# Kernel optimization log

Measured on AMD Instinct MI355X. Metric: run time of the kernel, lower is better.

## Reference

```python
import jax, jax.numpy as jnp
import numpy as np

V = 32000   # input_size (vocab)
H = 768     # hidden_size
C = 256     # condition_size
HC = H + C  # h_c_size
L = 2048    # sequence length


def _lstm_step(x, h, c, W_ih, W_hh, b_ih, b_hh):
    # PyTorch LSTM gate order: i, f, g, o
    gates = x @ W_ih.T + b_ih + h @ W_hh.T + b_hh  # [4*HC]
    i, f, g, o = jnp.split(gates, 4)
    c_new = jax.nn.sigmoid(f) * c + jax.nn.sigmoid(i) * jnp.tanh(g)
    h_new = jax.nn.sigmoid(o) * jnp.tanh(c_new)
    return h_new, c_new


def setup_inputs() -> dict:
    key = jax.random.key(0)
    ks = iter(jax.random.split(key, 40))
    p = lambda shape: (jax.random.normal(next(ks), shape, dtype=jnp.float32) * 0.02)
    inp = {
        "input": jax.random.randint(next(ks), (1, L), 0, V, dtype=jnp.int64),
        "condition": jax.random.randint(next(ks), (1,), 0, 4, dtype=jnp.int64),
        "eps_h": jax.random.normal(next(ks), (H,), dtype=jnp.float32),
        "eps_c": jax.random.normal(next(ks), (H,), dtype=jnp.float32),
        "kld_weight": jax.random.uniform(next(ks), (1,), dtype=jnp.float32),
        # encoder params
        "enc_embed": p((V, HC)),
        "enc_cond_embed": p((4, C)),
        "enc_W_ih": p((4 * HC, HC)), "enc_W_hh": p((4 * HC, HC)),
        "enc_b_ih": p((4 * HC,)), "enc_b_hh": p((4 * HC,)),
        "fc_mh_w": p((H, HC)), "fc_mh_b": p((H,)),
        "fc_lh_w": p((H, HC)), "fc_lh_b": p((H,)),
        "fc_mc_w": p((H, HC)), "fc_mc_b": p((H,)),
        "fc_lc_w": p((H, HC)), "fc_lc_b": p((H,)),
        # decoder params
        "dec_embed": p((V, HC)),
        "dec_cond_embed": p((4, C)),
        "dec_W_ih": p((4 * HC, HC)), "dec_W_hh": p((4 * HC, HC)),
        "dec_b_ih": p((4 * HC,)), "dec_b_hh": p((4 * HC,)),
        "fc_h_w": p((H, HC)), "fc_h_b": p((H,)),
        "fc_c_w": p((H, HC)), "fc_c_b": p((H,)),
        "out_w": p((V, HC)), "out_b": p((V,)),
    }
    return inp


def reference(input, condition, eps_h, eps_c, kld_weight,
              enc_embed, enc_cond_embed, enc_W_ih, enc_W_hh, enc_b_ih, enc_b_hh,
              fc_mh_w, fc_mh_b, fc_lh_w, fc_lh_b, fc_mc_w, fc_mc_b, fc_lc_w, fc_lc_b,
              dec_embed, dec_cond_embed, dec_W_ih, dec_W_hh, dec_b_ih, dec_b_hh,
              fc_h_w, fc_h_b, fc_c_w, fc_c_b, out_w, out_b):
    tokens = input[0]          # [L]
    cond = condition[0]

    # ---- Encoder over tokens[1:-1] ----
    x_seq = enc_embed[tokens[1:-1]]              # [L-2, HC]
    c_emb = enc_cond_embed[cond]                 # [C]
    h0 = jnp.concatenate([jnp.zeros((H,), jnp.float32), c_emb])  # [HC]
    c0 = h0

    def enc_step(carry, x):
        h, c = carry
        h, c = _lstm_step(x, h, c, enc_W_ih, enc_W_hh, enc_b_ih, enc_b_hh)
        return (h, c), None

    (hT, cT), _ = jax.lax.scan(enc_step, (h0, c0), x_seq)

    m_h = hT @ fc_mh_w.T + fc_mh_b
    lv_h = hT @ fc_lh_w.T + fc_lh_b
    z_h = eps_h * jnp.exp(lv_h * 0.5) + m_h      # [H]
    m_c = cT @ fc_mc_w.T + fc_mc_b
    lv_c = cT @ fc_lc_w.T + fc_lc_b
    z_c = eps_c * jnp.exp(lv_c * 0.5) + m_c

    kl_h = 0.5 * jnp.sum(m_h ** 2 + jnp.exp(lv_h) - 1.0 - lv_h)
    kl_c = 0.5 * jnp.sum(m_c ** 2 + jnp.exp(lv_c) - 1.0 - lv_c)

    # ---- Decoder, teacher forcing over L-1 steps ----
    dec_x = dec_embed[tokens[:-1]]               # [L-1, HC]
    targets = tokens[1:]                         # [L-1]
    cd = dec_cond_embed[cond]                    # [C]

    def dec_step(carry, xt):
        h, c = carry                             # [H], [H]
        x, tgt = xt
        hc = jnp.concatenate([h, cd])            # [HC]
        cc = jnp.concatenate([c, cd])
        h_new, c_new = _lstm_step(x, hc, cc, dec_W_ih, dec_W_hh, dec_b_ih, dec_b_hh)
        logits = h_new @ out_w.T + out_b         # [V]
        ce = -jax.nn.log_softmax(logits)[tgt]
        h2 = h_new @ fc_h_w.T + fc_h_b
        c2 = c_new @ fc_c_w.T + fc_c_b
        return (h2, c2), ce

    _, ces = jax.lax.scan(dec_step, (z_h, z_c), (dec_x, targets))
    reconst = jnp.mean(ces)
    loss = reconst + (kl_h + kl_c) * kld_weight[0]
    return jnp.stack([loss, reconst, kl_h, kl_c])
```

## Files before the change

### kernel.cpp

```cpp
#include <hip/hip_runtime.h>
#include <math.h>

#define VSZ 32000
#define Hh  768
#define Cc  256
#define HCd 1024
#define G4  4096
#define NSE 2046
#define NSD 2047

#define EB 64
#define ET 512
#define FGRID 256

typedef __attribute__((ext_vector_type(4))) unsigned uint4v;
typedef __attribute__((ext_vector_type(2))) unsigned uint2v;
typedef __attribute__((ext_vector_type(8))) short bf16x8;
typedef __attribute__((ext_vector_type(4))) float f32x4;

__device__ __forceinline__ float sigmoidf_(float x){ return 1.0f/(1.0f+expf(-x)); }

__device__ __forceinline__ float wave_reduce(float v){
#pragma unroll
  for(int o=32;o;o>>=1) v += __shfl_xor(v,o,64);
  return v;
}
__device__ __forceinline__ float redl0(float v){
  int x;
  x=__builtin_amdgcn_update_dpp(0,__float_as_int(v),0xB1,0xf,0xf,true); v+=__int_as_float(x);
  x=__builtin_amdgcn_update_dpp(0,__float_as_int(v),0x4E,0xf,0xf,true); v+=__int_as_float(x);
  v+=__int_as_float(__builtin_amdgcn_ds_swizzle(__float_as_int(v),0x101F));
  v+=__int_as_float(__builtin_amdgcn_ds_swizzle(__float_as_int(v),0x201F));
  v+=__int_as_float(__builtin_amdgcn_ds_swizzle(__float_as_int(v),0x401F));
  v+=__int_as_float(__builtin_amdgcn_readlane(__float_as_int(v),32));
  return v;
}

__device__ __forceinline__ uint2v ld_uc2(const unsigned* p){
  uint2v r;
  asm volatile("global_load_dwordx2 %0, %1, off sc0 sc1\n\ts_waitcnt vmcnt(0)"
               : "=v"(r) : "v"(p) : "memory");
  return r;
}
__device__ __forceinline__ uint4v ld_uc4(const unsigned* p){
  uint4v r;
  asm volatile("global_load_dwordx4 %0, %1, off sc0 sc1\n\ts_waitcnt vmcnt(0)"
               : "=v"(r) : "v"(p) : "memory");
  return r;
}
__device__ __forceinline__ void st_uc2(unsigned* p, uint2v v){
  asm volatile("global_store_dwordx2 %0, %1, off sc0 sc1" :: "v"(p), "v"(v) : "memory");
}
__device__ __forceinline__ void st_uc4(unsigned* p, uint4v v){
  asm volatile("global_store_dwordx4 %0, %1, off sc0 sc1" :: "v"(p), "v"(v) : "memory");
}

__device__ __forceinline__ unsigned pk_bf16(float a, float b){
  unsigned ua=__float_as_uint(a); ua += 0x7fffu + ((ua>>16)&1u);
  unsigned ub=__float_as_uint(b); ub += 0x7fffu + ((ub>>16)&1u);
  return (ua>>16) | (ub & 0xffff0000u);
}

__global__ void k_init9(unsigned* estate, unsigned* dstate,
                        const float* __restrict__ cemb, const int* __restrict__ condp){
  int tid=threadIdx.x;
  int cond=condp[0];
  for(int i=tid;i<HCd;i+=256){
    float v=(i<Hh)?0.f:cemb[cond*Cc+(i-Hh)];
    estate[i]=__float_as_uint(v)&~1u;
    estate[HCd+i]=1u;
  }
  for(int i=tid;i<2*HCd;i+=256) dstate[i]=0u;
}

#define GBM 128
#define GBN 128
#define GBK 16
#define TBM 128
#define TBN 128
#define TBK 32

struct SmU {
  union {
    float hlds[2][HCd];
    struct { float As[GBK][GBM]; float Bs[GBK][GBN]; } wf;
    struct { ushort As[TBM*TBK]; ushort Bs[TBN*TBK]; } xd;
  } u;
};

__device__ void weff_unit(int u, const float* __restrict__ A,
    const float* __restrict__ B, float* __restrict__ Cm, SmU& sm, int tid){
  int m0=(u>>3)*GBM, n0=(u&7)*GBN;
  int tm=tid>>4, tn=tid&15;
  float acc[8][8]={};
  for(int k0=0;k0<Hh;k0+=GBK){
    if(tid<256){
#pragma unroll
      for(int uu=0;uu<2;uu++){
        int idx=tid*2+uu;
        int row=idx>>2, q=idx&3;
        float4 v=*(const float4*)(A+(size_t)(m0+row)*HCd + k0+q*4);
        sm.u.wf.As[q*4+0][row]=v.x; sm.u.wf.As[q*4+1][row]=v.y;
        sm.u.wf.As[q*4+2][row]=v.z; sm.u.wf.As[q*4+3][row]=v.w;
        int kk=idx>>5, nc=idx&31;
        float4 w=*(const float4*)(B+(size_t)(k0+kk)*HCd + n0+nc*4);
        *(float4*)&sm.u.wf.Bs[kk][nc*4]=w;
      }
    }
    __syncthreads();
    if(tid<256){
#pragma unroll
      for(int kk=0;kk<GBK;kk++){
        float a[8],b[8];
        *(float4*)&a[0]=*(float4*)&sm.u.wf.As[kk][tm*8]; *(float4*)&a[4]=*(float4*)&sm.u.wf.As[kk][tm*8+4];
        *(float4*)&b[0]=*(float4*)&sm.u.wf.Bs[kk][tn*8]; *(float4*)&b[4]=*(float4*)&sm.u.wf.Bs[kk][tn*8+4];
#pragma unroll
        for(int i=0;i<8;i++)
#pragma unroll
          for(int j=0;j<8;j++) acc[i][j]+=a[i]*b[j];
      }
    }
    __syncthreads();
  }
  if(tid<256){
#pragma unroll
    for(int i=0;i<8;i++)
#pragma unroll
      for(int j=0;j<8;j++)
        Cm[(size_t)(m0+tm*8+i)*HCd + n0+tn*8+j]=acc[i][j];
  }
}

__device__ void xdec_unit(int q, const float* __restrict__ emb,
    const float* __restrict__ Wih, const float* __restrict__ b1,
    const float* __restrict__ b2, const int* __restrict__ tok,
    float* __restrict__ X, SmU& sm, int tid){
  int m0=(q>>5)*TBM, n0=(q&31)*TBN;
  int wid=tid>>6, lane=tid&63;
  int wm=wid>>1, wn=wid&1;
  int r15=lane&15, g=lane>>4;
  f32x4 acc[4][4]={};
  int srow=tid>>1, shalf=tid&1;
  int arow=m0+srow;
  bool act=(tid<256);
  int atok=(act&&arow<NSD)?tok[arow]:0;
  const float* aptr=emb+(size_t)atok*HCd + shalf*16;
  const float* bptr=Wih+(size_t)(n0+srow)*HCd + shalf*16;
  bool aok=act&&(arow<NSD);
  float bj[4];
  if(act){
#pragma unroll
    for(int j=0;j<4;j++){ int n=n0+wn*64+j*16+r15; bj[j]=b1[n]+b2[n]; }
  }
  for(int k0=0;k0<HCd;k0+=TBK){
    if(act){
      float4 va0={0,0,0,0},va1={0,0,0,0},va2={0,0,0,0},va3={0,0,0,0};
      if(aok){
        va0=*(const float4*)(aptr+k0);   va1=*(const float4*)(aptr+k0+4);
        va2=*(const float4*)(aptr+k0+8); va3=*(const float4*)(aptr+k0+12);
      }
      float4 vb0=*(const float4*)(bptr+k0),   vb1=*(const float4*)(bptr+k0+4);
      float4 vb2=*(const float4*)(bptr+k0+8), vb3=*(const float4*)(bptr+k0+12);
      uint4v pa0={pk_bf16(va0.x,va0.y),pk_bf16(va0.z,va0.w),pk_bf16(va1.x,va1.y),pk_bf16(va1.z,va1.w)};
      uint4v pa1={pk_bf16(va2.x,va2.y),pk_bf16(va2.z,va2.w),pk_bf16(va3.x,va3.y),pk_bf16(va3.z,va3.w)};
      uint4v pb0={pk_bf16(vb0.x,vb0.y),pk_bf16(vb0.z,vb0.w),pk_bf16(vb1.x,vb1.y),pk_bf16(vb1.z,vb1.w)};
      uint4v pb1={pk_bf16(vb2.x,vb2.y),pk_bf16(vb2.z,vb2.w),pk_bf16(vb3.x,vb3.y),pk_bf16(vb3.z,vb3.w)};
      int sx=(srow>>1)&3;
      int u0=(shalf*2+0)^sx, u1=(shalf*2+1)^sx;
      *(uint4v*)&sm.u.xd.As[srow*32+u0*8]=pa0; *(uint4v*)&sm.u.xd.As[srow*32+u1*8]=pa1;
      *(uint4v*)&sm.u.xd.Bs[srow*32+u0*8]=pb0; *(uint4v*)&sm.u.xd.Bs[srow*32+u1*8]=pb1;
    }
    __syncthreads();
    if(act){
      bf16x8 af[4], bf[4];
#pragma unroll
      for(int i=0;i<4;i++){
        int ra=wm*64+i*16+r15;
        af[i]=*(const bf16x8*)&sm.u.xd.As[ra*32+((g^((ra>>1)&3))<<3)];
        int rb=wn*64+i*16+r15;
        bf[i]=*(const bf16x8*)&sm.u.xd.Bs[rb*32+((g^((rb>>1)&3))<<3)];
      }
#pragma unroll
      for(int i=0;i<4;i++)
#pragma unroll
        for(int j=0;j<4;j++)
          acc[i][j]=__builtin_amdgcn_mfma_f32_16x16x32_bf16(af[i],bf[j],acc[i][j],0,0,0);
    }
    __syncthreads();
  }
  if(act){
#pragma unroll
    for(int i=0;i<4;i++){
      int grow0=m0+wm*64+i*16+g*4;
#pragma unroll
      for(int j=0;j<4;j++){
        int gcol=n0+wn*64+j*16+r15;
#pragma unroll
        for(int r=0;r<4;r++){
          int grow=grow0+r;
          if(grow<NSD) X[(size_t)grow*G4+gcol]=acc[i][j][r]+bj[j];
        }
      }
    }
  }
}

__device__ void cvtb_unit(int i, const float* __restrict__ B,
    unsigned* __restrict__ Bb, int tid){
  size_t base=(size_t)i*128000u;
  for(size_t x=base+tid; x<base+128000u; x+=ET){
    float4 v=*(const float4*)(B+x*4);
    Bb[x*2]  =pk_bf16(v.x,v.y);
    Bb[x*2+1]=pk_bf16(v.z,v.w);
  }
}

__device__ void dconst_unit(int i, const float* __restrict__ Whh,
    const float* __restrict__ fhb, const float* __restrict__ cemb,
    int cond, float* __restrict__ cvec, int tid){
// ... 142 lines not shown
    int do_xdec, int do_cvtb)
{
  __shared__ SmU sm;
  const int tid=threadIdx.x, lane=tid&63, wv=tid>>6;
  const int bid=blockIdx.x;

  if(bid>=EB){
    int cond=condp[0];
    int n_x=do_xdec?512:0, n_c=do_cvtb?64:0;
    int total=16+256+n_x+n_c;
    for(int u=bid-EB; u<total; u+=FGRID-EB){
      if(u<16) dconst_unit(u,dWhh,fhb,dcemb,cond,cvec,tid);
      else if(u<272) weff_unit(u-16,dWhh,fhw,Weff,sm,tid);
      else if(u<272+n_x) xdec_unit(u-272,demb,dWih,dbih,dbhh,tok,XB,sm,tid);
      else cvtb_unit(u-272-n_x,outw,wB,tid);
      __syncthreads();
    }
    return;
  }

  const int wid=bid*8+wv;
  const int j0=wid*2, j1=j0+1;
  float w[8][16];
#pragma unroll
  for(int q=0;q<4;q++)
#pragma unroll
    for(int jj=0;jj<2;jj++){
      const float* p=Whh+(size_t)(q*HCd+j0+jj)*HCd+lane;
#pragma unroll
      for(int e=0;e<16;e++) w[q*2+jj][e]=p[(size_t)e*64];
    }
  float xg[8];
#pragma unroll
  for(int r=0;r<8;r++) xg[r]=Xg[(r>>1)*HCd+j0+(r&1)];
  float c0=0.f,c1=0.f;
  const int i0=tid*2, i1=i0+1;

  for(int s=1;s<=NSE;s++){
    uint2v v;
    unsigned* src=estate+((s-1)&1)*HCd;
    if(s==1){ v.x=src[i0]; v.y=src[i1]; }
    else{
      const unsigned expp=(unsigned)(((s-1)>>1)&1);
      for(;;){
        v=ld_uc2(src+i0);
        if((((v.x^expp)|(v.y^expp))&1u)==0u) break;
        __builtin_amdgcn_s_sleep(1);
      }
    }
    float* hl=sm.u.hlds[(s-1)&1];
    hl[i0]=__uint_as_float(v.x); hl[i1]=__uint_as_float(v.y);
    __syncthreads();
    if(s==1){ c0=hl[j0]; c1=hl[j1]; }
    float hseg[16];
#pragma unroll
    for(int e=0;e<16;e++) hseg[e]=hl[lane+64*e];
    float d[8];
#pragma unroll
    for(int r=0;r<8;r++){ float sacc=0.f;
#pragma unroll
      for(int e=0;e<16;e++) sacc+=w[r][e]*hseg[e];
      d[r]=sacc; }
#pragma unroll
    for(int r=0;r<8;r++) d[r]=redl0(d[r]);
    float gi0=d[0]+xg[0], gi1=d[1]+xg[1];
    float gf0=d[2]+xg[2], gf1=d[3]+xg[3];
    float gg0=d[4]+xg[4], gg1=d[5]+xg[5];
    float go0=d[6]+xg[6], go1=d[7]+xg[7];
    if(s<NSE){
      const float* px=Xg+(size_t)s*G4;
#pragma unroll
      for(int r=0;r<8;r++) xg[r]=px[(r>>1)*HCd+j0+(r&1)];
    }
    c0=sigmoidf_(gf0)*c0+sigmoidf_(gi0)*tanhf(gg0);
    float h0=sigmoidf_(go0)*tanhf(c0);
    c1=sigmoidf_(gf1)*c1+sigmoidf_(gi1)*tanhf(gg1);
    float h1=sigmoidf_(go1)*tanhf(c1);
    unsigned wpar=(unsigned)((s>>1)&1);
    if(lane==0){
      uint2v pk;
      pk.x=(__float_as_uint(h0)&~1u)|wpar;
      pk.y=(__float_as_uint(h1)&~1u)|wpar;
      st_uc2(estate+(s&1)*HCd+j0,pk);
      if(s==NSE){ hT[j0]=h0; hT[j1]=h1; cT[j0]=c0; cT[j1]=c1; }
    }
  }
}

__global__ __launch_bounds__(256) void k_head(
    const float* __restrict__ hT, const float* __restrict__ cT,
    const float* __restrict__ mhw, const float* __restrict__ mhb,
    const float* __restrict__ lhw, const float* __restrict__ lhb,
    const float* __restrict__ mcw, const float* __restrict__ mcb,
    const float* __restrict__ lcw, const float* __restrict__ lcb,
    const float* __restrict__ eps_h, const float* __restrict__ eps_c,
    const float* __restrict__ cemb, const int* __restrict__ condp,
    float* zh, float* zc, float* klh, float* klc)
{
  int i=blockIdx.x;
  int tid=threadIdx.x, lane=tid&63, wv=tid>>6;
  __shared__ float sm[4];
  const float* Wm=(wv==0)?mhw:(wv==1)?lhw:(wv==2)?mcw:lcw;
  const float* vec=(wv<2)?hT:cT;
  const float* row=Wm+(size_t)i*HCd;
  float s=0.f;
  for(int k=lane;k<HCd;k+=64) s+=row[k]*vec[k];
  s=wave_reduce(s);
  if(lane==0) sm[wv]=s;
  __syncthreads();
  if(tid==0){
    float mh=sm[0]+mhb[i], lh=sm[1]+lhb[i];
    float mc=sm[2]+mcb[i], lc=sm[3]+lcb[i];
    zh[i]=eps_h[i]*expf(lh*0.5f)+mh;
    zc[i]=eps_c[i]*expf(lc*0.5f)+mc;
    klh[i]=0.5f*(mh*mh+expf(lh)-1.f-lh);
    klc[i]=0.5f*(mc*mc+expf(lc)-1.f-lc);
    if(i<Cc){
      float cd=cemb[condp[0]*Cc+i];
      zh[Hh+i]=cd; zc[Hh+i]=cd;
    }
  }
}

__global__ __launch_bounds__(256) void k_dec0(
    const float* __restrict__ Xg, const float* __restrict__ WhhO,
    const float* __restrict__ zh, const float* __restrict__ zc,
    unsigned* dstate1, float* Hmat)
{
  int tid=threadIdx.x, lane=tid&63, wv=tid>>6;
  int j=blockIdx.x*4+wv;
  float hseg[16];
#pragma unroll
  for(int e=0;e<16;e++) hseg[e]=zh[lane+64*e];
  float g[4];
#pragma unroll
  for(int q=0;q<4;q++){
    const float* p=WhhO+(size_t)(q*HCd+j)*HCd+lane;
    float s=0.f;
#pragma unroll
    for(int e=0;e<16;e++) s+=p[(size_t)e*64]*hseg[e];
    s=wave_reduce(s);
    g[q]=s+Xg[q*HCd+j];
  }
  float cc=zc[j];
  float cn=sigmoidf_(g[1])*cc+sigmoidf_(g[0])*tanhf(g[2]);
  float hn=sigmoidf_(g[3])*tanhf(cn);
  if(lane==0){
    dstate1[2*j]  =__float_as_uint(hn)&~1u;
    dstate1[2*j+1]=__float_as_uint(cn)&~1u;
    Hmat[j]=hn;
  }
}

__global__ __launch_bounds__(ET,2) void k_dec9(
    const float* __restrict__ Xg, const float* __restrict__ Weff,
    const float* __restrict__ cvec,
    const float* __restrict__ fccw, const float* __restrict__ fccb,
    const float* __restrict__ cemb, const int* __restrict__ condp,
    unsigned* dstate, float* __restrict__ Hmat)
{
  __shared__ float hlds[2][HCd];
  __shared__ float clds[2][HCd];
  const int tid=threadIdx.x, lane=tid&63, wv=tid>>6;
  const int wid=blockIdx.x*8+wv;
  const int j0=wid*2, j1=j0+1;
  float w[8][16];
#pragma unroll
  for(int q=0;q<4;q++)
#pragma unroll
    for(int jj=0;jj<2;jj++){
      const float* p=Weff+(size_t)(q*HCd+j0+jj)*HCd+lane;
#pragma unroll
      for(int e=0;e<16;e++) w[q*2+jj][e]=p[(size_t)e*64];
    }
  const bool hasf=(j0<Hh);
  float fcc0[16], fcc1[16];
  if(hasf){
    const float* p0=fccw+(size_t)j0*HCd+lane;
    const float* p1=fccw+(size_t)j1*HCd+lane;
#pragma unroll
    for(int e=0;e<16;e++){ fcc0[e]=p0[(size_t)e*64]; fcc1[e]=p1[(size_t)e*64]; }
  } else {
#pragma unroll
    for(int e=0;e<16;e++){ fcc0[e]=0.f; fcc1[e]=0.f; }
  }
  float fb0=hasf?fccb[j0]:0.f, fb1=hasf?fccb[j1]:0.f;
  int cond=condp[0];
  float cd0=hasf?0.f:cemb[cond*Cc+(j0-Hh)];
  float cd1=hasf?0.f:cemb[cond*Cc+(j1-Hh)];
  float cv[8];
#pragma unroll
  for(int r=0;r<8;r++) cv[r]=cvec[(r>>1)*HCd+j0+(r&1)];
  float xg[8];
  { const float* px=Xg+(size_t)1*G4;
#pragma unroll
    for(int r=0;r<8;r++) xg[r]=px[(r>>1)*HCd+j0+(r&1)]; }
  const int i0=tid*2, i1=i0+1;

  for(int s=2;s<=NSD;s++){
    uint4v v;
    unsigned* st=dstate+((s-1)&1)*2*HCd;
    if(s==2){ v=*(const uint4v*)(st+4*tid); }
    else{
      const unsigned expp=(unsigned)(((s-1)>>1)&1);
      for(;;){
        v=ld_uc4(st+4*tid);
        if((((v.x^expp)|(v.y^expp)|(v.z^expp)|(v.w^expp))&1u)==0u) break;
        __builtin_amdgcn_s_sleep(1);
      }
    }
    float* hl=hlds[(s-1)&1]; float* cl=clds[(s-1)&1];
    hl[i0]=__uint_as_float(v.x); cl[i0]=__uint_as_float(v.y);
    hl[i1]=__uint_as_float(v.z); cl[i1]=__uint_as_float(v.w);
    __syncthreads();
    float hseg[16], cseg[16];
#pragma unroll
    for(int e=0;e<16;e++){ hseg[e]=hl[lane+64*e]; cseg[e]=cl[lane+64*e]; }
    float d[8]; float s8=0.f, s9=0.f;
#pragma unroll
    for(int r=0;r<8;r++){ float sacc=0.f;
#pragma unroll
      for(int e=0;e<16;e++) sacc+=w[r][e]*hseg[e];
      d[r]=sacc; }
#pragma unroll
    for(int r=0;r<8;r++) d[r]=redl0(d[r]);
    if(hasf){
#pragma unroll
      for(int e=0;e<16;e++){ s8+=fcc0[e]*cseg[e]; s9+=fcc1[e]*cseg[e]; }
      s8=redl0(s8); s9=redl0(s9);
    }
    float gi0=d[0]+xg[0]+cv[0], gi1=d[1]+xg[1]+cv[1];
    float gf0=d[2]+xg[2]+cv[2], gf1=d[3]+xg[3]+cv[3];
    float gg0=d[4]+xg[4]+cv[4], gg1=d[5]+xg[5]+cv[5];
    float go0=d[6]+xg[6]+cv[6], go1=d[7]+xg[7]+cv[7];
    if(s<NSD){
      const float* px=Xg+(size_t)s*G4;
#pragma unroll
      for(int r=0;r<8;r++) xg[r]=px[(r>>1)*HCd+j0+(r&1)];
    }
    float cc0=hasf?(s8+fb0):cd0;
    float cc1=hasf?(s9+fb1):cd1;
    float cn0=sigmoidf_(gf0)*cc0+sigmoidf_(gi0)*tanhf(gg0);
    float hn0=sigmoidf_(go0)*tanhf(cn0);
    float cn1=sigmoidf_(gf1)*cc1+sigmoidf_(gi1)*tanhf(gg1);
    float hn1=sigmoidf_(go1)*tanhf(cn1);
    unsigned wpar=(unsigned)((s>>1)&1);
    if(lane==0){
      uint4v pk;
      pk.x=(__float_as_uint(hn0)&~1u)|wpar;
      pk.y=(__float_as_uint(cn0)&~1u)|wpar;
      pk.z=(__float_as_uint(hn1)&~1u)|wpar;
      pk.w=(__float_as_uint(cn1)&~1u)|wpar;
      st_uc4(dstate+(s&1)*2*HCd+2*j0,pk);
      Hmat[(size_t)(s-1)*HCd+j0]=hn0; Hmat[(size_t)(s-1)*HCd+j1]=hn1;
    }
  }
}

__global__ __launch_bounds__(256) void k_gemm2(
    const float* __restrict__ A, const ushort* __restrict__ Bb,
    const float* __restrict__ bias, float* __restrict__ Cm, int M)
{
  __shared__ ushort As[TBM*TBK];
  __shared__ ushort Bs[TBN*TBK];
  int tid=threadIdx.x;
  int m0=blockIdx.x*TBM, n0=blockIdx.y*TBN;
  int wid=tid>>6, lane=tid&63;
  int wm=wid>>1, wn=wid&1;
  int r15=lane&15, g=lane>>4;
  f32x4 acc[4][4]={};
  int srow=tid>>1, shalf=tid&1;
  const float*  aptr=A +(size_t)(m0+srow)*HCd + shalf*16;
  const ushort* bptr=Bb+(size_t)(n0+srow)*HCd + shalf*16;
  bool aok=(m0+srow)<M;
  float bj[4];
#pragma unroll
  for(int j=0;j<4;j++) bj[j]=bias[n0+wn*64+j*16+r15];

  for(int k0=0;k0<HCd;k0+=TBK){
    float4 va0={0,0,0,0},va1={0,0,0,0},va2={0,0,0,0},va3={0,0,0,0};
    if(aok){
      va0=*(const float4*)(aptr+k0);   va1=*(const float4*)(aptr+k0+4);
      va2=*(const float4*)(aptr+k0+8); va3=*(const float4*)(aptr+k0+12);
    }
    uint4v qb0=*(const uint4v*)(bptr+k0);
    uint4v qb1=*(const uint4v*)(bptr+k0+8);
    uint4v pa0={pk_bf16(va0.x,va0.y),pk_bf16(va0.z,va0.w),pk_bf16(va1.x,va1.y),pk_bf16(va1.z,va1.w)};
    uint4v pa1={pk_bf16(va2.x,va2.y),pk_bf16(va2.z,va2.w),pk_bf16(va3.x,va3.y),pk_bf16(va3.z,va3.w)};
    int sx=(srow>>1)&3;
    int u0=(shalf*2+0)^sx, u1=(shalf*2+1)^sx;
    *(uint4v*)&As[srow*32+u0*8]=pa0; *(uint4v*)&As[srow*32+u1*8]=pa1;
    *(uint4v*)&Bs[srow*32+u0*8]=qb0; *(uint4v*)&Bs[srow*32+u1*8]=qb1;
    __syncthreads();
    bf16x8 af[4], bf[4];
#pragma unroll
    for(int i=0;i<4;i++){
      int ra=wm*64+i*16+r15;
      af[i]=*(const bf16x8*)&As[ra*32+((g^((ra>>1)&3))<<3)];
      int rb=wn*64+i*16+r15;
      bf[i]=*(const bf16x8*)&Bs[rb*32+((g^((rb>>1)&3))<<3)];
    }
#pragma unroll
    for(int i=0;i<4;i++)
#pragma unroll
      for(int j=0;j<4;j++)
        acc[i][j]=__builtin_amdgcn_mfma_f32_16x16x32_bf16(af[i],bf[j],acc[i][j],0,0,0);
    __syncthreads();
  }
#pragma unroll
  for(int i=0;i<4;i++){
    int grow0=m0+wm*64+i*16+g*4;
#pragma unroll
    for(int j=0;j<4;j++){
      int gcol=n0+wn*64+j*16+r15;
#pragma unroll
      for(int r=0;r<4;r++){
        int grow=grow0+r;
        if(grow<M) Cm[(size_t)grow*VSZ+gcol]=acc[i][j][r]+bj[j];
      }
    }
  }
}

__global__ __launch_bounds__(256) void k_gemm_mfma(
    const float* __restrict__ A, const float* __restrict__ B,
    const float* __restrict__ bias, float* __restrict__ Cm, int M)
{
  __shared__ ushort As[TBM*TBK];
  __shared__ ushort Bs[TBN*TBK];
  int tid=threadIdx.x;
  int m0=blockIdx.x*TBM, n0=blockIdx.y*TBN;
  int wid=tid>>6, lane=tid&63;
  int wm=wid>>1, wn=wid&1;
  int r15=lane&15, g=lane>>4;
  f32x4 acc[4][4]={};
  int srow=tid>>1, shalf=tid&1;
  const float* aptr=A+(size_t)(m0+srow)*HCd + shalf*16;
  const float* bptr=B+(size_t)(n0+srow)*HCd + shalf*16;
  bool aok=(m0+srow)<M;
  float bj[4];
#pragma unroll
  for(int j=0;j<4;j++) bj[j]=bias[n0+wn*64+j*16+r15];
  for(int k0=0;k0<HCd;k0+=TBK){
    float4 va0={0,0,0,0},va1={0,0,0,0},va2={0,0,0,0},va3={0,0,0,0};
    if(aok){
      va0=*(const float4*)(aptr+k0);   va1=*(const float4*)(aptr+k0+4);
      va2=*(const float4*)(aptr+k0+8); va3=*(const float4*)(aptr+k0+12);
    }
    float4 vb0=*(const float4*)(bptr+k0),   vb1=*(const float4*)(bptr+k0+4);
    float4 vb2=*(const float4*)(bptr+k0+8), vb3=*(const float4*)(bptr+k0+12);
    uint4v pa0={pk_bf16(va0.x,va0.y),pk_bf16(va0.z,va0.w),pk_bf16(va1.x,va1.y),pk_bf16(va1.z,va1.w)};
    uint4v pa1={pk_bf16(va2.x,va2.y),pk_bf16(va2.z,va2.w),pk_bf16(va3.x,va3.y),pk_bf16(va3.z,va3.w)};
    uint4v pb0={pk_bf16(vb0.x,vb0.y),pk_bf16(vb0.z,vb0.w),pk_bf16(vb1.x,vb1.y),pk_bf16(vb1.z,vb1.w)};
    uint4v pb1={pk_bf16(vb2.x,vb2.y),pk_bf16(vb2.z,vb2.w),pk_bf16(vb3.x,vb3.y),pk_bf16(vb3.z,vb3.w)};
    int sx=(srow>>1)&3;
    int u0=(shalf*2+0)^sx, u1=(shalf*2+1)^sx;
    *(uint4v*)&As[srow*32+u0*8]=pa0; *(uint4v*)&As[srow*32+u1*8]=pa1;
    *(uint4v*)&Bs[srow*32+u0*8]=pb0; *(uint4v*)&Bs[srow*32+u1*8]=pb1;
    __syncthreads();
    bf16x8 af[4], bf[4];
#pragma unroll
    for(int i=0;i<4;i++){
      int ra=wm*64+i*16+r15;
      af[i]=*(const bf16x8*)&As[ra*32+((g^((ra>>1)&3))<<3)];
      int rb=wn*64+i*16+r15;
      bf[i]=*(const bf16x8*)&Bs[rb*32+((g^((rb>>1)&3))<<3)];
    }
#pragma unroll
    for(int i=0;i<4;i++)
#pragma unroll
      for(int j=0;j<4;j++)
        acc[i][j]=__builtin_amdgcn_mfma_f32_16x16x32_bf16(af[i],bf[j],acc[i][j],0,0,0);
    __syncthreads();
  }
#pragma unroll
  for(int i=0;i<4;i++){
    int grow0=m0+wm*64+i*16+g*4;
#pragma unroll
    for(int j=0;j<4;j++){
      int gcol=n0+wn*64+j*16+r15;
#pragma unroll
      for(int r=0;r<4;r++){
        int grow=grow0+r;
        if(grow<M) Cm[(size_t)grow*VSZ+gcol]=acc[i][j][r]+bj[j];
      }
    }
  }
}

__global__ __launch_bounds__(256) void k_ce(const float* __restrict__ logits,
    const int* __restrict__ tok, int base, float* __restrict__ ce)
{
  int r=blockIdx.x;
  const float* row=logits+(size_t)r*VSZ;
  int tid=threadIdx.x, lane=tid&63, wv=tid>>6;
  float m=-1e30f, s=0.f;
  for(int i=tid;i<VSZ;i+=256){
    float v=row[i];
    if(v>m){ s=s*__expf(m-v)+1.f; m=v; }
    else s+=__expf(v-m);
  }
#pragma unroll
  for(int o=32;o;o>>=1){
    float mo=__shfl_xor(m,o,64), so=__shfl_xor(s,o,64);
    float mn=fmaxf(m,mo);
    s=s*__expf(m-mn)+so*__expf(mo-mn);
    m=mn;
  }
  __shared__ float smm[4], sms[4];
  if(lane==0){ smm[wv]=m; sms[wv]=s; }
  __syncthreads();
  if(tid==0){
    float M2=fmaxf(fmaxf(smm[0],smm[1]),fmaxf(smm[2],smm[3]));
    float S2=sms[0]*__expf(smm[0]-M2)+sms[1]*__expf(smm[1]-M2)
            +sms[2]*__expf(smm[2]-M2)+sms[3]*__expf(smm[3]-M2);
    int tgt=tok[base+r+1];
    ce[base+r]=M2+logf(S2)-row[tgt];
  }
}

__global__ __launch_bounds__(256) void k_final(const float* __restrict__ ce,
    const float* __restrict__ klh, const float* __restrict__ klc,
    const float* __restrict__ kldw, float* __restrict__ outp)
{
  int tid=threadIdx.x, lane=tid&63, wv=tid>>6;
  float s0=0,s1=0,s2=0;
  for(int i=tid;i<NSD;i+=256) s0+=ce[i];
  for(int i=tid;i<Hh;i+=256){ s1+=klh[i]; s2+=klc[i]; }
  s0=wave_reduce(s0); s1=wave_reduce(s1); s2=wave_reduce(s2);
  __shared__ float sm[3][4];
  if(lane==0){ sm[0][wv]=s0; sm[1][wv]=s1; sm[2][wv]=s2; }
  __syncthreads();
  if(tid==0){
    float ces=sm[0][0]+sm[0][1]+sm[0][2]+sm[0][3];
    float kh =sm[1][0]+sm[1][1]+sm[1][2]+sm[1][3];
    float kc =sm[2][0]+sm[2][1]+sm[2][2]+sm[2][3];
    float rec=ces/(float)NSD;
    outp[0]=rec+(kh+kc)*kldw[0];
    outp[1]=rec; outp[2]=kh; outp[3]=kc;
  }
}

extern "C" void kernel_launch(void* const* d_in, const int* in_sizes, int n_in,
                              void* d_out, int out_size, void* d_ws, size_t ws_size,
                              hipStream_t stream) {
  const int*   tok   =(const int*)  d_in[0];
  const int*   cond  =(const int*)  d_in[1];
  const float* eps_h =(const float*)d_in[2];
  const float* eps_c =(const float*)d_in[3];
  const float* kldw  =(const float*)d_in[4];
  const float* enc_embed=(const float*)d_in[5];
  const float* enc_cemb =(const float*)d_in[6];
  const float* enc_Wih  =(const float*)d_in[7];
  const float* enc_Whh  =(const float*)d_in[8];
  const float* enc_bih  =(const float*)d_in[9];
  const float* enc_bhh  =(const float*)d_in[10];
  const float* fc_mh_w=(const float*)d_in[11];
  const float* fc_mh_b=(const float*)d_in[12];
  const float* fc_lh_w=(const float*)d_in[13];
  const float* fc_lh_b=(const float*)d_in[14];
  const float* fc_mc_w=(const float*)d_in[15];
  const float* fc_mc_b=(const float*)d_in[16];
  const float* fc_lc_w=(const float*)d_in[17];
  const float* fc_lc_b=(const float*)d_in[18];
  const float* dec_embed=(const float*)d_in[19];
  const float* dec_cemb =(const float*)d_in[20];
  const float* dec_Wih  =(const float*)d_in[21];
  const float* dec_Whh  =(const float*)d_in[22];
  const float* dec_bih  =(const float*)d_in[23];
  const float* dec_bhh  =(const float*)d_in[24];
  const float* fc_h_w=(const float*)d_in[25];
  const float* fc_h_b=(const float*)d_in[26];
  const float* fc_c_w=(const float*)d_in[27];
  const float* fc_c_b=(const float*)d_in[28];
  const float* out_w=(const float*)d_in[29];
  const float* out_b=(const float*)d_in[30];

  float* ws=(float*)d_ws;
  size_t off=0;
  unsigned* estate=(unsigned*)(ws+off); off+=2*HCd;
  unsigned* dstate=(unsigned*)(ws+off); off+=4*HCd;
  float* cvec=ws+off; off+=G4;
  float* Weff=ws+off; off+=(size_t)G4*HCd;
  float* hT  =ws+off; off+=HCd;
  float* cT  =ws+off; off+=HCd;
  float* zh  =ws+off; off+=HCd;
  float* zc  =ws+off; off+=HCd;
  float* klh =ws+off; off+=Hh;
  float* klc =ws+off; off+=Hh;
  float* Hmat=ws+off; off+=(size_t)NSD*HCd;
  float* ce  =ws+off; off+=2048;
  size_t avail=ws_size/4;
  size_t xa_sz=(size_t)NSE*G4, xb_sz=(size_t)NSD*G4;
  size_t wb_sz=(size_t)VSZ*HCd/2;
  float* XA=ws+off;
  bool dual=(off+xa_sz+xb_sz)<=avail;
  float* XB=dual?(XA+xa_sz):XA;
  bool wbok=dual && (off+xa_sz+xb_sz+wb_sz)<=avail;
  unsigned* wB=(unsigned*)(XB+xb_sz);
  size_t region=(avail>off)?(avail-off):0;
  int chunk;
  if(dual){
    chunk=(int)((xa_sz+xb_sz)/(size_t)VSZ); if(chunk>512)chunk=512;
  } else {
    chunk=256;
    if((size_t)chunk*VSZ>region){ chunk=(int)(region/(size_t)VSZ); if(chunk<1)chunk=1; }
  }
  float* lbuf=XA;

  k_init9<<<1,256,0,stream>>>(estate,dstate,enc_cemb,cond);
  { dim3 g((NSE+GBM-1)/GBM, G4/GBN);
    k_xgemm<<<g,256,0,stream>>>(enc_embed,enc_Wih,enc_bih,enc_bhh,tok,1,NSE,XA); }
  k_encF<<<FGRID,ET,0,stream>>>(XA,enc_Whh,estate,hT,cT,
                                dec_Whh,fc_h_w,Weff,
                                dec_embed,dec_Wih,dec_bih,dec_bhh,tok,XB,
                                out_w,wB,fc_h_b,dec_cemb,cond,cvec,
                                dual?1:0, wbok?1:0);
  k_head<<<Hh,256,0,stream>>>(hT,cT,fc_mh_w,fc_mh_b,fc_lh_w,fc_lh_b,
                              fc_mc_w,fc_mc_b,fc_lc_w,fc_lc_b,
                              eps_h,eps_c,dec_cemb,cond,zh,zc,klh,klc);
  if(!dual){
    dim3 g((NSD+TBM-1)/TBM, G4/TBN);
    k_xgemm_mfma<<<g,256,0,stream>>>(dec_embed,dec_Wih,dec_bih,dec_bhh,tok,NSD,XB);
  }
  k_dec0<<<256,256,0,stream>>>(XB,dec_Whh,zh,zc,dstate+2*HCd,Hmat);
  k_dec9<<<EB,ET,0,stream>>>(XB,Weff,cvec,fc_c_w,fc_c_b,dec_cemb,cond,dstate,Hmat);
  for(int base=0;base<NSD;base+=chunk){
    int rows=NSD-base; if(rows>chunk) rows=chunk;
    dim3 g((rows+TBM-1)/TBM, VSZ/TBN);
    if(wbok) k_gemm2<<<g,256,0,stream>>>(Hmat+(size_t)base*HCd,(const ushort*)wB,out_b,lbuf,rows);
    else     k_gemm_mfma<<<g,256,0,stream>>>(Hmat+(size_t)base*HCd,out_w,out_b,lbuf,rows);
    k_ce<<<rows,256,0,stream>>>(lbuf,tok,base,ce);
  }
  k_final<<<1,256,0,stream>>>(ce,klh,klc,kldw,(float*)d_out);
}
```

Before: 13.53 ms.

## Overlap decoder scan with fused vocab GEMM and online softmax via progress flags

Replaces the sequential decoder recurrence kernel and the chunked vocab-projection GEMM plus CE kernels with one persistent kernel. The first 64 blocks run the recurrence and publish per-block progress counters. The remaining blocks spin on those counters and compute the output logits tiles for rows already finished. They fuse bias, target-logit extraction and a partial log-sum-exp per tile, so the full logits matrix is never written. A small merge kernel then combines the partial max and sum values into the cross-entropy. The gain depends on all 256 blocks being co-resident, and the GEMM blocks contend with the latency-critical scan for memory bandwidth.

```diff
diff --git a/kernel.cpp b/kernel.cpp
--- a/kernel.cpp
+++ b/kernel.cpp
@@ -12,6 +12,7 @@
 #define EB 64
 #define ET 512
 #define FGRID 256
+#define NCT 125
 
 typedef __attribute__((ext_vector_type(4))) unsigned uint4v;
 typedef __attribute__((ext_vector_type(2))) unsigned uint2v;
@@ -23,6 +24,11 @@
 __device__ __forceinline__ float wave_reduce(float v){
 #pragma unroll
   for(int o=32;o;o>>=1) v += __shfl_xor(v,o,64);
+  return v;
+}
+__device__ __forceinline__ unsigned wave_min_u(unsigned v){
+#pragma unroll
+  for(int o=32;o;o>>=1){ unsigned x=__shfl_xor(v,o,64); v=(x<v)?x:v; }
   return v;
 }
 __device__ __forceinline__ float redl0(float v){
@@ -36,6 +42,12 @@
   return v;
 }
 
+__device__ __forceinline__ unsigned ld_uc1(const unsigned* p){
+  unsigned r;
+  asm volatile("global_load_dword %0, %1, off sc0 sc1\n\ts_waitcnt vmcnt(0)"
+               : "=v"(r) : "v"(p) : "memory");
+  return r;
+}
 __device__ __forceinline__ uint2v ld_uc2(const unsigned* p){
   uint2v r;
   asm volatile("global_load_dwordx2 %0, %1, off sc0 sc1\n\ts_waitcnt vmcnt(0)"
@@ -48,6 +60,9 @@
                : "=v"(r) : "v"(p) : "memory");
   return r;
 }
+__device__ __forceinline__ void st_uc1(unsigned* p, unsigned v){
+  asm volatile("global_store_dword %0, %1, off sc0 sc1" :: "v"(p), "v"(v) : "memory");
+}
 __device__ __forceinline__ void st_uc2(unsigned* p, uint2v v){
   asm volatile("global_store_dwordx2 %0, %1, off sc0 sc1" :: "v"(p), "v"(v) : "memory");
 }
@@ -61,10 +76,11 @@
   return (ua>>16) | (ub & 0xffff0000u);
 }
 
-__global__ void k_init9(unsigned* estate, unsigned* dstate,
-                        const float* __restrict__ cemb, const int* __restrict__ condp){
+__global__ void k_init12(unsigned* prog, unsigned* estate, unsigned* dstate,
+                         const float* __restrict__ cemb, const int* __restrict__ condp){
   int tid=threadIdx.x;
   int cond=condp[0];
+  for(int i=tid;i<4096;i+=256) prog[i]=0u;
   for(int i=tid;i<HCd;i+=256){
     float v=(i<Hh)?0.f:cemb[cond*Cc+(i-Hh)];
     estate[i]=__float_as_uint(v)&~1u;
@@ -513,6 +529,244 @@
   }
 }
 
+struct SmD {
+  union {
+    struct { float hl[2][HCd]; float cl[2][HCd]; } scan;
+    struct { ushort As[128*32]; ushort Bs[256*32];
+             float smM[128][4]; float smL[128][4]; int tgt[128]; } h;
+  } u;
+};
+
+__global__ __launch_bounds__(ET) void k_decF(
+    const float* __restrict__ Xg, const float* __restrict__ Weff,
+    const float* __restrict__ cvec,
+    const float* __restrict__ fccw, const float* __restrict__ fccb,
+    const float* __restrict__ cemb, const int* __restrict__ condp,
+    unsigned* dstate, float* __restrict__ Hmat, unsigned* prog,
+    const ushort* __restrict__ wB, const float* __restrict__ outb,
+    const int* __restrict__ tok,
+    float* __restrict__ pm, float* __restrict__ pl, float* __restrict__ tgtlog)
+{
+  __shared__ SmD smem;
+  const int tid=threadIdx.x, lane=tid&63, wv=tid>>6;
+  const int bid=blockIdx.x;
+
+  if(bid<EB){
+    const int wid=bid*8+wv;
+    const int j0=wid*2, j1=j0+1;
+    float w[8][16];
+#pragma unroll
+    for(int q=0;q<4;q++)
+#pragma unroll
+      for(int jj=0;jj<2;jj++){
+        const float* p=Weff+(size_t)(q*HCd+j0+jj)*HCd+lane;
+#pragma unroll
+        for(int e=0;e<16;e++) w[q*2+jj][e]=p[(size_t)e*64];
+      }
+    const bool hasf=(j0<Hh);
+    float fcc0[16], fcc1[16];
+    if(hasf){
+      const float* p0=fccw+(size_t)j0*HCd+lane;
+      const float* p1=fccw+(size_t)j1*HCd+lane;
+#pragma unroll
+      for(int e=0;e<16;e++){ fcc0[e]=p0[(size_t)e*64]; fcc1[e]=p1[(size_t)e*64]; }
+    } else {
+#pragma unroll
+      for(int e=0;e<16;e++){ fcc0[e]=0.f; fcc1[e]=0.f; }
+    }
+    float fb0=hasf?fccb[j0]:0.f, fb1=hasf?fccb[j1]:0.f;
+    int cond=condp[0];
+    float cd0=hasf?0.f:cemb[cond*Cc+(j0-Hh)];
+    float cd1=hasf?0.f:cemb[cond*Cc+(j1-Hh)];
+    float cv[8];
+#pragma unroll
+    for(int r=0;r<8;r++) cv[r]=cvec[(r>>1)*HCd+j0+(r&1)];
+    float xg[8];
+    { const float* px=Xg+(size_t)1*G4;
+#pragma unroll
+      for(int r=0;r<8;r++) xg[r]=px[(r>>1)*HCd+j0+(r&1)]; }
+    const int i0=tid*2, i1=i0+1;
+
+    for(int s=2;s<=NSD;s++){
+      uint4v v;
+      unsigned* st=dstate+((s-1)&1)*2*HCd;
+      if(s==2){ v=*(const uint4v*)(st+4*tid); }
+      else{
+        const unsigned expp=(unsigned)(((s-1)>>1)&1);
+        for(;;){
+          v=ld_uc4(st+4*tid);
+          if((((v.x^expp)|(v.y^expp)|(v.z^expp)|(v.w^expp))&1u)==0u) break;
+          __builtin_amdgcn_s_sleep(1);
+        }
+      }
+      float* hl=smem.u.scan.hl[(s-1)&1]; float* cl=smem.u.scan.cl[(s-1)&1];
+      hl[i0]=__uint_as_float(v.x); cl[i0]=__uint_as_float(v.y);
+      hl[i1]=__uint_as_float(v.z); cl[i1]=__uint_as_float(v.w);
+      __syncthreads();
+      if(tid==0) st_uc1(prog+bid*64,(unsigned)(s-2));
+      float hseg[16], cseg[16];
+#pragma unroll
+      for(int e=0;e<16;e++){ hseg[e]=hl[lane+64*e]; cseg[e]=cl[lane+64*e]; }
+      float d[8]; float s8=0.f, s9=0.f;
+#pragma unroll
+      for(int r=0;r<8;r++){ float sacc=0.f;
+#pragma unroll
+        for(int e=0;e<16;e++) sacc+=w[r][e]*hseg[e];
+        d[r]=sacc; }
+#pragma unroll
+      for(int r=0;r<8;r++) d[r]=redl0(d[r]);
+      if(hasf){
+#pragma unroll
+        for(int e=0;e<16;e++){ s8+=fcc0[e]*cseg[e]; s9+=fcc1[e]*cseg[e]; }
+        s8=redl0(s8); s9=redl0(s9);
+      }
+      float gi0=d[0]+xg[0]+cv[0], gi1=d[1]+xg[1]+cv[1];
+      float gf0=d[2]+xg[2]+cv[2], gf1=d[3]+xg[3]+cv[3];
+      float gg0=d[4]+xg[4]+cv[4], gg1=d[5]+xg[5]+cv[5];
+      float go0=d[6]+xg[6]+cv[6], go1=d[7]+xg[7]+cv[7];
+      if(s<NSD){
+        const float* px=Xg+(size_t)s*G4;
+#pragma unroll
+        for(int r=0;r<8;r++) xg[r]=px[(r>>1)*HCd+j0+(r&1)];
+      }
+      float cc0=hasf?(s8+fb0):cd0;
+      float cc1=hasf?(s9+fb1):cd1;
+      float cn0=sigmoidf_(gf0)*cc0+sigmoidf_(gi0)*tanhf(gg0);
+      float hn0=sigmoidf_(go0)*tanhf(cn0);
+      float cn1=sigmoidf_(gf1)*cc1+sigmoidf_(gi1)*tanhf(gg1);
+      float hn1=sigmoidf_(go1)*tanhf(cn1);
+      unsigned wpar=(unsigned)((s>>1)&1);
+      if(lane==0){
+        uint4v pk;
+        pk.x=(__float_as_uint(hn0)&~1u)|wpar;
+        pk.y=(__float_as_uint(cn0)&~1u)|wpar;
+        pk.z=(__float_as_uint(hn1)&~1u)|wpar;
+        pk.w=(__float_as_uint(cn1)&~1u)|wpar;
+        st_uc4(dstate+(s&1)*2*HCd+2*j0,pk);
+        uint2v hm; hm.x=__float_as_uint(hn0); hm.y=__float_as_uint(hn1);
+        st_uc2((unsigned*)(Hmat+(size_t)(s-1)*HCd+j0),hm);
+      }
+    }
+    asm volatile("s_waitcnt vmcnt(0)");
+    __syncthreads();
+    if(tid==0) st_uc1(prog+bid*64,(unsigned)(NSD-1));
+    return;
+  }
+
+  const int hb=bid-EB;
+  const int wid=tid>>6;
+  const int r15=lane&15, g=lane>>4;
+  const int wm=wid>>2, wn=wid&3;
+  const int srA=tid>>2, shA=tid&3;
+  const int srB=tid>>1, shB=tid&1;
+
+  for(int u=hb; u<8*2*NCT; u+=FGRID-EB){
+    int chunk=u/(2*NCT), t=u%(2*NCT);
+    int rt=t/NCT, ct=t%NCT;
+    int m0=chunk*256+rt*128, n0=ct*256;
+    unsigned need=(unsigned)((m0+127<NSD)?(m0+127):(NSD-1));
+    if(wv==0){
+      for(;;){
+        unsigned pv=ld_uc1(prog+lane*64);
+        if(wave_min_u(pv)>=need) break;
+        __builtin_amdgcn_s_sleep(32);
+      }
+    }
+    if(tid<128){
+      int grow=m0+tid;
+      smem.u.h.tgt[tid]=(grow<NSD)?tok[grow+1]:-1;
+    }
+    __syncthreads();
+
+    f32x4 acc[4][4]={};
+    const float*  aptr=Hmat+(size_t)(m0+srA)*HCd + shA*8;
+    const ushort* bptr=wB  +(size_t)(n0+srB)*HCd + shB*16;
+    bool aok=(m0+srA)<NSD;
+    for(int k0=0;k0<HCd;k0+=32){
+      float4 va0={0,0,0,0}, va1={0,0,0,0};
+      if(aok){ va0=*(const float4*)(aptr+k0); va1=*(const float4*)(aptr+k0+4); }
+      uint4v pa={pk_bf16(va0.x,va0.y),pk_bf16(va0.z,va0.w),pk_bf16(va1.x,va1.y),pk_bf16(va1.z,va1.w)};
+      int sxA=(srA>>1)&3;
+      *(uint4v*)&smem.u.h.As[srA*32+(shA^sxA)*8]=pa;
+      uint4v qb0=*(const uint4v*)(bptr+k0);
+      uint4v qb1=*(const uint4v*)(bptr+k0+8);
+      int sxB=(srB>>1)&3;
+      int u0=(shB*2+0)^sxB, u1=(shB*2+1)^sxB;
+      *(uint4v*)&smem.u.h.Bs[srB*32+u0*8]=qb0;
+      *(uint4v*)&smem.u.h.Bs[srB*32+u1*8]=qb1;
+      __syncthreads();
+      bf16x8 af[4], bf[4];
+#pragma unroll
+      for(int i=0;i<4;i++){
+        int ra=wm*64+i*16+r15;
+        af[i]=*(const bf16x8*)&smem.u.h.As[ra*32+((g^((ra>>1)&3))<<3)];
+        int rb=wn*64+i*16+r15;
+        bf[i]=*(const bf16x8*)&smem.u.h.Bs[rb*32+((g^((rb>>1)&3))<<3)];
+      }
+#pragma unroll
+      for(int i=0;i<4;i++)
+#pragma unroll
+        for(int j=0;j<4;j++)
+          acc[i][j]=__builtin_amdgcn_mfma_f32_16x16x32_bf16(af[i],bf[j],acc[i][j],0,0,0);
+      __syncthreads();
+    }
+    float bj[4];
+#pragma unroll
+    for(int j=0;j<4;j++) bj[j]=outb[n0+wn*64+j*16+r15];
+#pragma unroll
+    for(int i=0;i<4;i++)
+#pragma unroll
+    for(int r=0;r<4;r++){
+      int rloc=wm*64+i*16+g*4+r;
+      int tg=smem.u.h.tgt[rloc];
+      float vv[4];
+#pragma unroll
+      for(int j=0;j<4;j++){
+        vv[j]=acc[i][j][r]+bj[j];
+        if(n0+wn*64+j*16+r15==tg) tgtlog[m0+rloc]=vv[j];
+      }
+      float mloc=fmaxf(fmaxf(vv[0],vv[1]),fmaxf(vv[2],vv[3]));
+      float lloc=__expf(vv[0]-mloc)+__expf(vv[1]-mloc)+__expf(vv[2]-mloc)+__expf(vv[3]-mloc);
+#pragma unroll
+      for(int o=1;o<16;o<<=1){
+        float mo=__shfl_xor(mloc,o,64), lo=__shfl_xor(lloc,o,64);
+        float mn=fmaxf(mloc,mo);
+        lloc=lloc*__expf(mloc-mn)+lo*__expf(mo-mn);
+        mloc=mn;
+      }
+      if(r15==0){ smem.u.h.smM[rloc][wn]=mloc; smem.u.h.smL[rloc][wn]=lloc; }
+    }
+    __syncthreads();
+    if(tid<128){
+      int grow=m0+tid;
+      if(grow<NSD){
+        float M=-3e38f;
+#pragma unroll
+        for(int q2=0;q2<4;q2++) M=fmaxf(M,smem.u.h.smM[tid][q2]);
+        float L=0.f;
+#pragma unroll
+        for(int q2=0;q2<4;q2++) L+=smem.u.h.smL[tid][q2]*__expf(smem.u.h.smM[tid][q2]-M);
+        pm[(size_t)grow*NCT+ct]=M;
+        pl[(size_t)grow*NCT+ct]=L;
+      }
+    }
+    __syncthreads();
+  }
+}
+
+__global__ __launch_bounds__(256) void k_cemerge(const float* __restrict__ pm,
+    const float* __restrict__ pl, const float* __restrict__ tgtlog,
+    float* __restrict__ ce)
+{
+  int grow=blockIdx.x*256+threadIdx.x;
+  if(grow>=NSD) return;
+  float M=-3e38f;
+  for(int c=0;c<NCT;c++) M=fmaxf(M,pm[(size_t)grow*NCT+c]);
+  float L=0.f;
+  for(int c=0;c<NCT;c++) L+=pl[(size_t)grow*NCT+c]*__expf(pm[(size_t)grow*NCT+c]-M);
+  ce[grow]=M+logf(L)-tgtlog[grow];
+}
+
 __global__ __launch_bounds__(ET,2) void k_dec9(
     const float* __restrict__ Xg, const float* __restrict__ Weff,
     const float* __restrict__ cvec,
@@ -614,71 +868,6 @@
       pk.w=(__float_as_uint(cn1)&~1u)|wpar;
       st_uc4(dstate+(s&1)*2*HCd+2*j0,pk);
       Hmat[(size_t)(s-1)*HCd+j0]=hn0; Hmat[(size_t)(s-1)*HCd+j1]=hn1;
-    }
-  }
-}
-
-__global__ __launch_bounds__(256) void k_gemm2(
-    const float* __restrict__ A, const ushort* __restrict__ Bb,
-    const float* __restrict__ bias, float* __restrict__ Cm, int M)
-{
-  __shared__ ushort As[TBM*TBK];
-  __shared__ ushort Bs[TBN*TBK];
-  int tid=threadIdx.x;
-  int m0=blockIdx.x*TBM, n0=blockIdx.y*TBN;
-  int wid=tid>>6, lane=tid&63;
-  int wm=wid>>1, wn=wid&1;
-  int r15=lane&15, g=lane>>4;
-  f32x4 acc[4][4]={};
-  int srow=tid>>1, shalf=tid&1;
-  const float*  aptr=A +(size_t)(m0+srow)*HCd + shalf*16;
-  const ushort* bptr=Bb+(size_t)(n0+srow)*HCd + shalf*16;
-  bool aok=(m0+srow)<M;
-  float bj[4];
-#pragma unroll
-  for(int j=0;j<4;j++) bj[j]=bias[n0+wn*64+j*16+r15];
-
-  for(int k0=0;k0<HCd;k0+=TBK){
-    float4 va0={0,0,0,0},va1={0,0,0,0},va2={0,0,0,0},va3={0,0,0,0};
-    if(aok){
-      va0=*(const float4*)(aptr+k0);   va1=*(const float4*)(aptr+k0+4);
-      va2=*(const float4*)(aptr+k0+8); va3=*(const float4*)(aptr+k0+12);
-    }
-    uint4v qb0=*(const uint4v*)(bptr+k0);
-    uint4v qb1=*(const uint4v*)(bptr+k0+8);
-    uint4v pa0={pk_bf16(va0.x,va0.y),pk_bf16(va0.z,va0.w),pk_bf16(va1.x,va1.y),pk_bf16(va1.z,va1.w)};
-    uint4v pa1={pk_bf16(va2.x,va2.y),pk_bf16(va2.z,va2.w),pk_bf16(va3.x,va3.y),pk_bf16(va3.z,va3.w)};
-    int sx=(srow>>1)&3;
-    int u0=(shalf*2+0)^sx, u1=(shalf*2+1)^sx;
-    *(uint4v*)&As[srow*32+u0*8]=pa0; *(uint4v*)&As[srow*32+u1*8]=pa1;
-    *(uint4v*)&Bs[srow*32+u0*8]=qb0; *(uint4v*)&Bs[srow*32+u1*8]=qb1;
-    __syncthreads();
-    bf16x8 af[4], bf[4];
-#pragma unroll
-    for(int i=0;i<4;i++){
-      int ra=wm*64+i*16+r15;
-      af[i]=*(const bf16x8*)&As[ra*32+((g^((ra>>1)&3))<<3)];
-      int rb=wn*64+i*16+r15;
-      bf[i]=*(const bf16x8*)&Bs[rb*32+((g^((rb>>1)&3))<<3)];
-    }
-#pragma unroll
-    for(int i=0;i<4;i++)
-#pragma unroll
-      for(int j=0;j<4;j++)
-        acc[i][j]=__builtin_amdgcn_mfma_f32_16x16x32_bf16(af[i],bf[j],acc[i][j],0,0,0);
-    __syncthreads();
-  }
-#pragma unroll
-  for(int i=0;i<4;i++){
-    int grow0=m0+wm*64+i*16+g*4;
-#pragma unroll
-    for(int j=0;j<4;j++){
-      int gcol=n0+wn*64+j*16+r15;
-#pragma unroll
-      for(int r=0;r<4;r++){
-        int grow=grow0+r;
-        if(grow<M) Cm[(size_t)grow*VSZ+gcol]=acc[i][j][r]+bj[j];
-      }
     }
   }
 }
@@ -839,6 +1028,7 @@
 
   float* ws=(float*)d_ws;
   size_t off=0;
+  unsigned* prog  =(unsigned*)(ws+off); off+=4096;
   unsigned* estate=(unsigned*)(ws+off); off+=2*HCd;
   unsigned* dstate=(unsigned*)(ws+off); off+=4*HCd;
   float* cvec=ws+off; off+=G4;
@@ -851,6 +1041,9 @@
   float* klc =ws+off; off+=Hh;
   float* Hmat=ws+off; off+=(size_t)NSD*HCd;
   float* ce  =ws+off; off+=2048;
+  float* pm  =ws+off; off+=(size_t)2048*NCT;
+  float* pl  =ws+off; off+=(size_t)2048*NCT;
+  float* tgtlog=ws+off; off+=2048;
   size_t avail=ws_size/4;
   size_t xa_sz=(size_t)NSE*G4, xb_sz=(size_t)NSD*G4;
   size_t wb_sz=(size_t)VSZ*HCd/2;
@@ -860,16 +1053,13 @@
   bool wbok=dual && (off+xa_sz+xb_sz+wb_sz)<=avail;
   unsigned* wB=(unsigned*)(XB+xb_sz);
   size_t region=(avail>off)?(avail-off):0;
-  int chunk;
-  if(dual){
-    chunk=(int)((xa_sz+xb_sz)/(size_t)VSZ); if(chunk>512)chunk=512;
-  } else {
-    chunk=256;
+  int chunk=256;
+  if(!dual){
     if((size_t)chunk*VSZ>region){ chunk=(int)(region/(size_t)VSZ); if(chunk<1)chunk=1; }
   }
   float* lbuf=XA;
 
-  k_init9<<<1,256,0,stream>>>(estate,dstate,enc_cemb,cond);
+  k_init12<<<1,256,0,stream>>>(prog,estate,dstate,enc_cemb,cond);
   { dim3 g((NSE+GBM-1)/GBM, G4/GBN);
     k_xgemm<<<g,256,0,stream>>>(enc_embed,enc_Wih,enc_bih,enc_bhh,tok,1,NSE,XA); }
   k_encF<<<FGRID,ET,0,stream>>>(XA,enc_Whh,estate,hT,cT,
@@ -885,13 +1075,19 @@
     k_xgemm_mfma<<<g,256,0,stream>>>(dec_embed,dec_Wih,dec_bih,dec_bhh,tok,NSD,XB);
   }
   k_dec0<<<256,256,0,stream>>>(XB,dec_Whh,zh,zc,dstate+2*HCd,Hmat);
-  k_dec9<<<EB,ET,0,stream>>>(XB,Weff,cvec,fc_c_w,fc_c_b,dec_cemb,cond,dstate,Hmat);
-  for(int base=0;base<NSD;base+=chunk){
-    int rows=NSD-base; if(rows>chunk) rows=chunk;
-    dim3 g((rows+TBM-1)/TBM, VSZ/TBN);
-    if(wbok) k_gemm2<<<g,256,0,stream>>>(Hmat+(size_t)base*HCd,(const ushort*)wB,out_b,lbuf,rows);
-    else     k_gemm_mfma<<<g,256,0,stream>>>(Hmat+(size_t)base*HCd,out_w,out_b,lbuf,rows);
-    k_ce<<<rows,256,0,stream>>>(lbuf,tok,base,ce);
+  if(dual&&wbok){
+    k_decF<<<FGRID,ET,0,stream>>>(XB,Weff,cvec,fc_c_w,fc_c_b,dec_cemb,cond,
+                                  dstate,Hmat,prog,(const ushort*)wB,out_b,tok,
+                                  pm,pl,tgtlog);
+    k_cemerge<<<(NSD+255)/256,256,0,stream>>>(pm,pl,tgtlog,ce);
+  } else {
+    k_dec9<<<EB,ET,0,stream>>>(XB,Weff,cvec,fc_c_w,fc_c_b,dec_cemb,cond,dstate,Hmat);
+    for(int base=0;base<NSD;base+=chunk){
+      int rows=NSD-base; if(rows>chunk) rows=chunk;
+      dim3 g((rows+TBM-1)/TBM, VSZ/TBN);
+      k_gemm_mfma<<<g,256,0,stream>>>(Hmat+(size_t)base*HCd,out_w,out_b,lbuf,rows);
+      k_ce<<<rows,256,0,stream>>>(lbuf,tok,base,ce);
+    }
   }
   k_final<<<1,256,0,stream>>>(ce,klh,klc,kldw,(float*)d_out);
 }
```

New measurement: 12.99 ms. 4.0% less time.
